# Kernel tuning notes

Hardware: AMD Instinct MI355X
Metric: run time of the kernel (lower is better)

The kernel has to match this reference:

```python
import jax, jax.numpy as jnp
import numpy as np

N_NODES = 100000
N_EDGES = 600000
IN_SIZE = 128
OUT_SIZE = 128
N_GRAPHS = 100
BN_EPS = 1e-5


def setup_inputs() -> dict:
    key = jax.random.key(0)
    ks = jax.random.split(key, 8)
    h = jax.random.normal(ks[0], (N_NODES, IN_SIZE), dtype=jnp.float32)
    norm = jax.random.uniform(ks[1], (N_NODES, 1), dtype=jnp.float32)
    src = jax.random.randint(ks[2], (N_EDGES,), 0, N_NODES, dtype=jnp.int32)
    dst = jax.random.randint(ks[3], (N_EDGES,), 0, N_NODES, dtype=jnp.int32)
    graph_ids = jnp.sort(jax.random.randint(ks[4], (N_NODES,), 0, N_GRAPHS, dtype=jnp.int32))
    # Linear + BatchNorm params
    W = jax.random.normal(ks[5], (IN_SIZE, OUT_SIZE), dtype=jnp.float32) / np.sqrt(IN_SIZE)
    b = jnp.zeros((OUT_SIZE,), dtype=jnp.float32)
    gamma = jnp.ones((OUT_SIZE,), dtype=jnp.float32)
    beta = jnp.zeros((OUT_SIZE,), dtype=jnp.float32)
    return {"h": h, "norm": norm, "W": W, "b": b, "gamma": gamma, "beta": beta,
            "src": src, "dst": dst, "graph_ids": graph_ids}


def reference(h, norm, W, b, gamma, beta, src, dst, graph_ids):
    # pre-normalize, scatter-sum over edges (copy_src + sum), post-normalize
    x = h * norm                                            # [N, in]
    agg = jax.ops.segment_sum(x[src], dst, num_segments=N_NODES)  # SpMM
    x = agg * norm
    # linear + relu
    x = jax.nn.relu(jnp.dot(x, W) + b)                      # [N, out]
    # BatchNorm1d (training-mode: batch mean, biased variance)
    mean = jnp.mean(x, axis=0)
    var = jnp.mean(jnp.square(x - mean), axis=0)
    x = (x - mean) * jax.lax.rsqrt(var + BN_EPS) * gamma + beta
    # sum_nodes pooling per graph
    phis = jax.ops.segment_sum(x, graph_ids, num_segments=N_GRAPHS)  # [G, out]
    return (x, phis)
```

## Files before the change

### kernel.cpp

```cpp
#include <hip/hip_runtime.h>
#include <hip/hip_bf16.h>

#define N_NODES 100000
#define N_EDGES 600000
#define CH 128
#define N_GRAPHS 100
#define BN_EPS 1e-5f
#define NBUCKET 16
#define CAP 16
#define OVFCAP 8192
#define EDGE_BLOCKS 2344
#define GEMM_BLOCKS 782
#define GATHER_BLOCKS 1024
#define ZERO_INTS (N_NODES + 2 * NBUCKET * CH + 4)
#define ZERO_BLOCKS 407
#define PHIS_BLOCKS 50
#define WT_BLOCKS 64

typedef __bf16 bf16x8 __attribute__((ext_vector_type(8)));
typedef float f32x4 __attribute__((ext_vector_type(4)));

__device__ __forceinline__ ushort f2bf(float f) {
    union { float f; unsigned u; } x; x.f = f;
    unsigned u = x.u;
    unsigned r = (u + 0x7fffu + ((u >> 16) & 1u)) >> 16;
    return (ushort)r;
}
__device__ __forceinline__ float bflo(unsigned p) { return __builtin_bit_cast(float, p << 16); }
__device__ __forceinline__ float bfhi(unsigned p) { return __builtin_bit_cast(float, p & 0xffff0000u); }

__global__ __launch_bounds__(256) void k_prep(const float* __restrict__ W,
        int* __restrict__ zbase, ushort* __restrict__ Wt, float* __restrict__ phis) {
    unsigned bid = blockIdx.x;
    int tid = threadIdx.x;
    if (bid < ZERO_BLOCKS) {
        int i = bid * 256 + tid;
        if (i < ZERO_INTS) zbase[i] = 0;
    } else if (bid < ZERO_BLOCKS + PHIS_BLOCKS) {
        int i = (bid - ZERO_BLOCKS) * 256 + tid;
        phis[i] = 0.f;
    } else {
        int t = (bid - ZERO_BLOCKS - PHIS_BLOCKS) * 256 + tid;
        int k = t >> 7, o = t & 127;
        Wt[o * CH + k] = f2bf(W[t]);
    }
}

__global__ __launch_bounds__(256) void k_fill(const int* __restrict__ src,
        const int* __restrict__ dst, int* __restrict__ cnt,
        int* __restrict__ ovfcur, int* __restrict__ ovf, int* __restrict__ esrc) {
    int e = blockIdx.x * 256 + threadIdx.x;
    if (e < N_EDGES) {
        int d = dst[e], s = src[e];
        int slot = atomicAdd(&cnt[d], 1);
        if (slot < CAP) esrc[d * CAP + slot] = s;
        else { int p = atomicAdd(ovfcur, 1); if (p < OVFCAP) { ovf[2*p] = d; ovf[2*p+1] = s; } }
    }
}

__device__ __forceinline__ bf16x8 mk_b(const float* __restrict__ hrow, int k,
                                       float nm, bool valid) {
    union { bf16x8 v; ushort u[8]; } r;
    if (valid) {
        float4 p = *(const float4*)(hrow + k);
        float4 q = *(const float4*)(hrow + k + 4);
        r.u[0] = f2bf(p.x * nm); r.u[1] = f2bf(p.y * nm);
        r.u[2] = f2bf(p.z * nm); r.u[3] = f2bf(p.w * nm);
        r.u[4] = f2bf(q.x * nm); r.u[5] = f2bf(q.y * nm);
        r.u[6] = f2bf(q.z * nm); r.u[7] = f2bf(q.w * nm);
    } else {
        #pragma unroll
        for (int i = 0; i < 8; i++) r.u[i] = 0;
    }
    return r.v;
}

__global__ __launch_bounds__(256) void k_zgemm(const float* __restrict__ h,
        const float* __restrict__ norm, const ushort* __restrict__ Wt,
        ushort* __restrict__ z16) {
    int tid = threadIdx.x;
    int gb = blockIdx.x;
    int w = tid >> 6, L = tid & 63;
    int c15 = L & 15, quad = L >> 4;
    int nb = gb * 128 + w * 32;
    int n0 = nb + c15, n1 = nb + 16 + c15;
    bool v0 = n0 < N_NODES, v1 = n1 < N_NODES;
    float nm0 = v0 ? norm[n0] : 0.f;
    float nm1 = v1 ? norm[n1] : 0.f;
    const float* h0 = h + (size_t)n0 * CH;
    const float* h1 = h + (size_t)n1 * CH;

    f32x4 acc0[8] = {}, acc1[8] = {};
    #pragma unroll
    for (int kt = 0; kt < 4; kt++) {
        int k = kt * 32 + quad * 8;
        bf16x8 b0 = mk_b(h0, k, nm0, v0);
        bf16x8 b1 = mk_b(h1, k, nm1, v1);
        #pragma unroll
        for (int ot = 0; ot < 8; ot++) {
            bf16x8 a = *(const bf16x8*)(Wt + (size_t)(ot * 16 + c15) * CH + k);
            acc0[ot] = __builtin_amdgcn_mfma_f32_16x16x32_bf16(a, b0, acc0[ot], 0, 0, 0);
            acc1[ot] = __builtin_amdgcn_mfma_f32_16x16x32_bf16(a, b1, acc1[ot], 0, 0, 0);
        }
    }

    if (v0) {
        ushort* zr = z16 + (size_t)n0 * CH;
        #pragma unroll
        for (int ot = 0; ot < 8; ot++) {
            uint2 dv;
            dv.x = (unsigned)f2bf(acc0[ot][0]) | ((unsigned)f2bf(acc0[ot][1]) << 16);
            dv.y = (unsigned)f2bf(acc0[ot][2]) | ((unsigned)f2bf(acc0[ot][3]) << 16);
            *(uint2*)(zr + ot * 16 + quad * 4) = dv;
        }
    }
    if (v1) {
        ushort* zr = z16 + (size_t)n1 * CH;
        #pragma unroll
        for (int ot = 0; ot < 8; ot++) {
            uint2 dv;
            dv.x = (unsigned)f2bf(acc1[ot][0]) | ((unsigned)f2bf(acc1[ot][1]) << 16);
            dv.y = (unsigned)f2bf(acc1[ot][2]) | ((unsigned)f2bf(acc1[ot][3]) << 16);
            *(uint2*)(zr + ot * 16 + quad * 4) = dv;
        }
    }
}

__global__ __launch_bounds__(256) void k_gather(const ushort* __restrict__ z16,
        const float* __restrict__ norm, const int* __restrict__ cnt,
        const int* __restrict__ esrc, const int* __restrict__ ovfcur,
        const int* __restrict__ ovf, const float* __restrict__ bias,
        ushort* __restrict__ y16, float* __restrict__ psum, float* __restrict__ psq) {
    __shared__ float sred[2][16][CH];

    int tid = threadIdx.x;
    int cg = tid & 15, rl = tid >> 4;
    int c = cg * 8;
    float4 b0 = *(const float4*)(bias + c), b1 = *(const float4*)(bias + c + 4);
    float s8[8] = {}, q8[8] = {};
    int no = min(*ovfcur, OVFCAP);

    for (int n = blockIdx.x * 16 + rl; n < N_NODES; n += GATHER_BLOCKS * 16) {
        int e = min(cnt[n], CAP);
        float nn = norm[n];
        int base = n * CAP;
        float a0=0.f,a1=0.f,a2=0.f,a3=0.f,a4=0.f,a5=0.f,a6=0.f,a7=0.f;
        int j = 0;
        for (; j + 4 <= e; j += 4) {
            int4 s4 = *(const int4*)(esrc + base + j);
            uint4 v0 = *(const uint4*)(z16 + (size_t)s4.x * CH + c);
            uint4 v1 = *(const uint4*)(z16 + (size_t)s4.y * CH + c);
            uint4 v2 = *(const uint4*)(z16 + (size_t)s4.z * CH + c);
            uint4 v3 = *(const uint4*)(z16 + (size_t)s4.w * CH + c);
            a0 += bflo(v0.x) + bflo(v1.x) + bflo(v2.x) + bflo(v3.x);
            a1 += bfhi(v0.x) + bfhi(v1.x) + bfhi(v2.x) + bfhi(v3.x);
            a2 += bflo(v0.y) + bflo(v1.y) + bflo(v2.y) + bflo(v3.y);
            a3 += bfhi(v0.y) + bfhi(v1.y) + bfhi(v2.y) + bfhi(v3.y);
            a4 += bflo(v0.z) + bflo(v1.z) + bflo(v2.z) + bflo(v3.z);
            a5 += bfhi(v0.z) + bfhi(v1.z) + bfhi(v2.z) + bfhi(v3.z);
            a6 += bflo(v0.w) + bflo(v1.w) + bflo(v2.w) + bflo(v3.w);
            a7 += bfhi(v0.w) + bfhi(v1.w) + bfhi(v2.w) + bfhi(v3.w);
        }
        for (; j < e; j++) {
            int s = esrc[base + j];
            uint4 v = *(const uint4*)(z16 + (size_t)s * CH + c);
            a0 += bflo(v.x); a1 += bfhi(v.x);
            a2 += bflo(v.y); a3 += bfhi(v.y);
            a4 += bflo(v.z); a5 += bfhi(v.z);
            a6 += bflo(v.w); a7 += bfhi(v.w);
        }
        if (no > 0) {
            for (int i = 0; i < no; i++) {
                if (ovf[2*i] == n) {
                    int s = ovf[2*i+1];
                    uint4 v = *(const uint4*)(z16 + (size_t)s * CH + c);
                    a0 += bflo(v.x); a1 += bfhi(v.x);
                    a2 += bflo(v.y); a3 += bfhi(v.y);
                    a4 += bflo(v.z); a5 += bfhi(v.z);
                    a6 += bflo(v.w); a7 += bfhi(v.w);
                }
            }
        }
        float f[8];
        f[0] = fmaxf(fmaf(a0, nn, b0.x), 0.f);
        f[1] = fmaxf(fmaf(a1, nn, b0.y), 0.f);
        f[2] = fmaxf(fmaf(a2, nn, b0.z), 0.f);
        f[3] = fmaxf(fmaf(a3, nn, b0.w), 0.f);
        f[4] = fmaxf(fmaf(a4, nn, b1.x), 0.f);
        f[5] = fmaxf(fmaf(a5, nn, b1.y), 0.f);
        f[6] = fmaxf(fmaf(a6, nn, b1.z), 0.f);
        f[7] = fmaxf(fmaf(a7, nn, b1.w), 0.f);
        uint4 o;
        o.x = (unsigned)f2bf(f[0]) | ((unsigned)f2bf(f[1]) << 16);
        o.y = (unsigned)f2bf(f[2]) | ((unsigned)f2bf(f[3]) << 16);
        o.z = (unsigned)f2bf(f[4]) | ((unsigned)f2bf(f[5]) << 16);
        o.w = (unsigned)f2bf(f[6]) | ((unsigned)f2bf(f[7]) << 16);
        *(uint4*)(y16 + (size_t)n * CH + c) = o;
        #pragma unroll
        for (int k = 0; k < 8; k++) { s8[k] += f[k]; q8[k] += f[k] * f[k]; }
    }

    *(float4*)&sred[0][rl][c]     = make_float4(s8[0], s8[1], s8[2], s8[3]);
    *(float4*)&sred[0][rl][c + 4] = make_float4(s8[4], s8[5], s8[6], s8[7]);
    *(float4*)&sred[1][rl][c]     = make_float4(q8[0], q8[1], q8[2], q8[3]);
    *(float4*)&sred[1][rl][c + 4] = make_float4(q8[4], q8[5], q8[6], q8[7]);
    __syncthreads();
    if (tid < 128) {
        float S = 0.f, Q = 0.f;
        #pragma unroll
        for (int k = 0; k < 16; k++) { S += sred[0][k][tid]; Q += sred[1][k][tid]; }
        int bucket = blockIdx.x & (NBUCKET - 1);
        atomicAdd(&psum[bucket * CH + tid], S);
        atomicAdd(&psq[bucket * CH + tid], Q);
    }
}

__global__ __launch_bounds__(256) void k_bnpool(const ushort* __restrict__ y16,
        const int* __restrict__ gids, const float* __restrict__ psum,
        const float* __restrict__ psq, const float* __restrict__ gamma,
        const float* __restrict__ beta, float* __restrict__ xout,
        float* __restrict__ phis) {
    __shared__ float smP[16][CH];
    __shared__ float ssc[CH], ssh[CH];

    int tid = threadIdx.x;
    if (tid < 128) {
        float S = 0.f, Q = 0.f;
        #pragma unroll
        for (int g = 0; g < NBUCKET; g++) { S += psum[g * CH + tid]; Q += psq[g * CH + tid]; }
        const float invN = 1.f / (float)N_NODES;
        float mean = S * invN;
        float var  = Q * invN - mean * mean;
        float sc   = gamma[tid] * rsqrtf(var + BN_EPS);
        ssc[tid] = sc;
        ssh[tid] = beta[tid] - mean * sc;
    }
    __syncthreads();

    int cg = tid & 15, rl = tid >> 4;
    int c = cg * 8;
    int r0 = blockIdx.x * 256;
    int rbase = r0 + rl * 16;

    float4 sc0 = *(const float4*)&ssc[c], sc1 = *(const float4*)&ssc[c + 4];
    float4 sh0 = *(const float4*)&ssh[c], sh1 = *(const float4*)&ssh[c + 4];

    bool fast = (r0 + 255 < N_NODES) && (gids[r0] == gids[r0 + 255]);

    if (fast) {
        float4 p0 = make_float4(0.f,0.f,0.f,0.f), p1 = make_float4(0.f,0.f,0.f,0.f);
        for (int j = 0; j < 16; j++) {
            int r = rbase + j;
            uint4 v = *(const uint4*)(y16 + (size_t)r * CH + c);
            float4 f0, f1;
            f0.x = fmaf(bflo(v.x), sc0.x, sh0.x); f0.y = fmaf(bfhi(v.x), sc0.y, sh0.y);
            f0.z = fmaf(bflo(v.y), sc0.z, sh0.z); f0.w = fmaf(bfhi(v.y), sc0.w, sh0.w);
            f1.x = fmaf(bflo(v.z), sc1.x, sh1.x); f1.y = fmaf(bfhi(v.z), sc1.y, sh1.y);
            f1.z = fmaf(bflo(v.w), sc1.z, sh1.z); f1.w = fmaf(bfhi(v.w), sc1.w, sh1.w);
            *(float4*)(xout + (size_t)r * CH + c) = f0;
            *(float4*)(xout + (size_t)r * CH + c + 4) = f1;
            p0.x += f0.x; p0.y += f0.y; p0.z += f0.z; p0.w += f0.w;
            p1.x += f1.x; p1.y += f1.y; p1.z += f1.z; p1.w += f1.w;
        }
        *(float4*)&smP[rl][c] = p0;
        *(float4*)&smP[rl][c + 4] = p1;
        __syncthreads();
        if (tid < 128) {
            int g = gids[r0];
            float S = 0.f;
            #pragma unroll
            for (int k = 0; k < 16; k++) S += smP[k][tid];
            atomicAdd(&phis[(size_t)g * CH + tid], S);
        }
    } else {
        float p[8] = {};
        int gprev = -1;
        for (int j = 0; j < 16; j++) {
            int r = rbase + j;
            if (r >= N_NODES) break;
            int g = gids[r];
            if (g != gprev) {
                if (gprev >= 0) {
                    #pragma unroll
                    for (int k = 0; k < 8; k++) {
                        atomicAdd(&phis[(size_t)gprev * CH + c + k], p[k]);
                        p[k] = 0.f;
                    }
                }
                gprev = g;
            }
            uint4 v = *(const uint4*)(y16 + (size_t)r * CH + c);
            float f[8];
            f[0] = fmaf(bflo(v.x), sc0.x, sh0.x); f[1] = fmaf(bfhi(v.x), sc0.y, sh0.y);
            f[2] = fmaf(bflo(v.y), sc0.z, sh0.z); f[3] = fmaf(bfhi(v.y), sc0.w, sh0.w);
            f[4] = fmaf(bflo(v.z), sc1.x, sh1.x); f[5] = fmaf(bfhi(v.z), sc1.y, sh1.y);
            f[6] = fmaf(bflo(v.w), sc1.z, sh1.z); f[7] = fmaf(bfhi(v.w), sc1.w, sh1.w);
            *(float4*)(xout + (size_t)r * CH + c) = make_float4(f[0], f[1], f[2], f[3]);
            *(float4*)(xout + (size_t)r * CH + c + 4) = make_float4(f[4], f[5], f[6], f[7]);
            #pragma unroll
            for (int k = 0; k < 8; k++) p[k] += f[k];
        }
        if (gprev >= 0) {
            #pragma unroll
            for (int k = 0; k < 8; k++)
                atomicAdd(&phis[(size_t)gprev * CH + c + k], p[k]);
        }
    }
}

extern "C" void kernel_launch(void* const* d_in, const int* in_sizes, int n_in,
                              void* d_out, int out_size, void* d_ws, size_t ws_size,
                              hipStream_t stream)
{
    const float* h     = (const float*)d_in[0];
    const float* norm  = (const float*)d_in[1];
    const float* W     = (const float*)d_in[2];
    const float* b     = (const float*)d_in[3];
    const float* gamma = (const float*)d_in[4];
    const float* beta  = (const float*)d_in[5];
    const int*   src   = (const int*)d_in[6];
    const int*   dst   = (const int*)d_in[7];
    const int*   gids  = (const int*)d_in[8];

    float* x_out = (float*)d_out;
    float* phis  = x_out + (size_t)N_NODES * CH;

    ushort* z16  = (ushort*)d_ws;
    ushort* y16  = z16 + (size_t)N_NODES * CH;
    ushort* Wt   = y16 + (size_t)N_NODES * CH;
    int*   cnt     = (int*)(Wt + CH * CH);
    float* psum    = (float*)(cnt + N_NODES);
    float* psq     = psum + NBUCKET * CH;
    int*   ovfcur  = (int*)(psq + NBUCKET * CH);
    int*   esrc    = ovfcur + 4;
    int*   ovf     = esrc + (size_t)N_NODES * CAP;

    k_prep<<<ZERO_BLOCKS + PHIS_BLOCKS + WT_BLOCKS, 256, 0, stream>>>(W, cnt, Wt, phis);
    k_fill<<<EDGE_BLOCKS, 256, 0, stream>>>(src, dst, cnt, ovfcur, ovf, esrc);
    k_zgemm<<<GEMM_BLOCKS, 256, 0, stream>>>(h, norm, Wt, z16);
    k_gather<<<GATHER_BLOCKS, 256, 0, stream>>>(
        z16, norm, cnt, esrc, ovfcur, ovf, b, y16, psum, psq);
    k_bnpool<<<(N_NODES + 255) / 256, 256, 0, stream>>>(
        y16, gids, psum, psq, gamma, beta, x_out, phis);
}
```

Baseline: 233.5 us.

## Shrink per-block work in GEMM and BN-pool, double gather grid, skip overflow scan

The GEMM kernel now has each wave handle 16 nodes instead of 32, doubling the grid. The BN/pool kernel covers 64 rows per block instead of 256 with unrolled loops, and the gather grid and stat buckets are doubled. Gather also scans the overflow list only for nodes whose edge count exceeds the cap, instead of every node whenever any overflow exists. The aim is more parallelism and less wasted overflow scanning, at the cost of more blocks, more atomics into phis, and more W reloads per node.

```diff
diff --git a/kernel.cpp b/kernel.cpp
--- a/kernel.cpp
+++ b/kernel.cpp
@@ -6,14 +6,15 @@
 #define CH 128
 #define N_GRAPHS 100
 #define BN_EPS 1e-5f
-#define NBUCKET 16
+#define NBUCKET 32
 #define CAP 16
 #define OVFCAP 8192
 #define EDGE_BLOCKS 2344
-#define GEMM_BLOCKS 782
-#define GATHER_BLOCKS 1024
+#define GEMM_BLOCKS 1563
+#define GATHER_BLOCKS 2048
+#define BN_BLOCKS 1563
 #define ZERO_INTS (N_NODES + 2 * NBUCKET * CH + 4)
-#define ZERO_BLOCKS 407
+#define ZERO_BLOCKS 423
 #define PHIS_BLOCKS 50
 #define WT_BLOCKS 64
 
@@ -79,28 +80,22 @@
         const float* __restrict__ norm, const ushort* __restrict__ Wt,
         ushort* __restrict__ z16) {
     int tid = threadIdx.x;
-    int gb = blockIdx.x;
     int w = tid >> 6, L = tid & 63;
     int c15 = L & 15, quad = L >> 4;
-    int nb = gb * 128 + w * 32;
-    int n0 = nb + c15, n1 = nb + 16 + c15;
-    bool v0 = n0 < N_NODES, v1 = n1 < N_NODES;
+    int n0 = blockIdx.x * 64 + w * 16 + c15;
+    bool v0 = n0 < N_NODES;
     float nm0 = v0 ? norm[n0] : 0.f;
-    float nm1 = v1 ? norm[n1] : 0.f;
     const float* h0 = h + (size_t)n0 * CH;
-    const float* h1 = h + (size_t)n1 * CH;
-
-    f32x4 acc0[8] = {}, acc1[8] = {};
+
+    f32x4 acc[8] = {};
     #pragma unroll
     for (int kt = 0; kt < 4; kt++) {
         int k = kt * 32 + quad * 8;
         bf16x8 b0 = mk_b(h0, k, nm0, v0);
-        bf16x8 b1 = mk_b(h1, k, nm1, v1);
         #pragma unroll
         for (int ot = 0; ot < 8; ot++) {
             bf16x8 a = *(const bf16x8*)(Wt + (size_t)(ot * 16 + c15) * CH + k);
-            acc0[ot] = __builtin_amdgcn_mfma_f32_16x16x32_bf16(a, b0, acc0[ot], 0, 0, 0);
-            acc1[ot] = __builtin_amdgcn_mfma_f32_16x16x32_bf16(a, b1, acc1[ot], 0, 0, 0);
+            acc[ot] = __builtin_amdgcn_mfma_f32_16x16x32_bf16(a, b0, acc[ot], 0, 0, 0);
         }
     }
 
@@ -109,18 +104,8 @@
         #pragma unroll
         for (int ot = 0; ot < 8; ot++) {
             uint2 dv;
-            dv.x = (unsigned)f2bf(acc0[ot][0]) | ((unsigned)f2bf(acc0[ot][1]) << 16);
-            dv.y = (unsigned)f2bf(acc0[ot][2]) | ((unsigned)f2bf(acc0[ot][3]) << 16);
-            *(uint2*)(zr + ot * 16 + quad * 4) = dv;
-        }
-    }
-    if (v1) {
-        ushort* zr = z16 + (size_t)n1 * CH;
-        #pragma unroll
-        for (int ot = 0; ot < 8; ot++) {
-            uint2 dv;
-            dv.x = (unsigned)f2bf(acc1[ot][0]) | ((unsigned)f2bf(acc1[ot][1]) << 16);
-            dv.y = (unsigned)f2bf(acc1[ot][2]) | ((unsigned)f2bf(acc1[ot][3]) << 16);
+            dv.x = (unsigned)f2bf(acc[ot][0]) | ((unsigned)f2bf(acc[ot][1]) << 16);
+            dv.y = (unsigned)f2bf(acc[ot][2]) | ((unsigned)f2bf(acc[ot][3]) << 16);
             *(uint2*)(zr + ot * 16 + quad * 4) = dv;
         }
     }
@@ -141,7 +126,8 @@
     int no = min(*ovfcur, OVFCAP);
 
     for (int n = blockIdx.x * 16 + rl; n < N_NODES; n += GATHER_BLOCKS * 16) {
-        int e = min(cnt[n], CAP);
+        int craw = cnt[n];
+        int e = min(craw, CAP);
         float nn = norm[n];
         int base = n * CAP;
         float a0=0.f,a1=0.f,a2=0.f,a3=0.f,a4=0.f,a5=0.f,a6=0.f,a7=0.f;
@@ -169,7 +155,7 @@
             a4 += bflo(v.z); a5 += bfhi(v.z);
             a6 += bflo(v.w); a7 += bfhi(v.w);
         }
-        if (no > 0) {
+        if (craw > CAP && no > 0) {
             for (int i = 0; i < no; i++) {
                 if (ovf[2*i] == n) {
                     int s = ovf[2*i+1];
@@ -239,17 +225,18 @@
 
     int cg = tid & 15, rl = tid >> 4;
     int c = cg * 8;
-    int r0 = blockIdx.x * 256;
-    int rbase = r0 + rl * 16;
+    int r0 = blockIdx.x * 64;
+    int rbase = r0 + rl * 4;
 
     float4 sc0 = *(const float4*)&ssc[c], sc1 = *(const float4*)&ssc[c + 4];
     float4 sh0 = *(const float4*)&ssh[c], sh1 = *(const float4*)&ssh[c + 4];
 
-    bool fast = (r0 + 255 < N_NODES) && (gids[r0] == gids[r0 + 255]);
+    bool fast = (r0 + 63 < N_NODES) && (gids[r0] == gids[r0 + 63]);
 
     if (fast) {
         float4 p0 = make_float4(0.f,0.f,0.f,0.f), p1 = make_float4(0.f,0.f,0.f,0.f);
-        for (int j = 0; j < 16; j++) {
+        #pragma unroll
+        for (int j = 0; j < 4; j++) {
             int r = rbase + j;
             uint4 v = *(const uint4*)(y16 + (size_t)r * CH + c);
             float4 f0, f1;
@@ -275,7 +262,8 @@
     } else {
         float p[8] = {};
         int gprev = -1;
-        for (int j = 0; j < 16; j++) {
+        #pragma unroll
+        for (int j = 0; j < 4; j++) {
             int r = rbase + j;
             if (r >= N_NODES) break;
             int g = gids[r];
@@ -340,6 +328,6 @@
     k_zgemm<<<GEMM_BLOCKS, 256, 0, stream>>>(h, norm, Wt, z16);
     k_gather<<<GATHER_BLOCKS, 256, 0, stream>>>(
         z16, norm, cnt, esrc, ovfcur, ovf, b, y16, psum, psq);
-    k_bnpool<<<(N_NODES + 255) / 256, 256, 0, stream>>>(
+    k_bnpool<<<BN_BLOCKS, 256, 0, stream>>>(
         y16, gids, psum, psq, gamma, beta, x_out, phis);
 }
```

After: 234.0 us. About the same (+0.2%).
